# Performance work log

Hardware: AMD Instinct MI355X
Metric: run time of the kernel (lower is better)

The kernel has to match this reference:

```python
import jax, jax.numpy as jnp
import numpy as np

NEG_SLOPE = 0.2
NUM_GRAPHS = 256


def _gatv2(x, src, dst, n_nodes, Wl, Wr, att, bias):
    # PyG GATv2Conv (heads=1): e_ij = att . leaky_relu(Wl x_j + Wr x_i)
    xl = x @ Wl                      # [N, C]
    xr = x @ Wr                      # [N, C]
    e = jnp.dot(jax.nn.leaky_relu(xl[src] + xr[dst], NEG_SLOPE), att)  # [E]
    # segment softmax over incoming edges of each target node
    m = jax.ops.segment_max(e, dst, num_segments=n_nodes)
    m = jnp.where(jnp.isfinite(m), m, 0.0)
    p = jnp.exp(e - m[dst])
    denom = jax.ops.segment_sum(p, dst, num_segments=n_nodes)
    alpha = p / jnp.maximum(denom[dst], 1e-16)
    out = jax.ops.segment_sum(alpha[:, None] * xl[src], dst, num_segments=n_nodes)
    return out + bias


def _add_self_loops(edge_index, n_nodes):
    loops = jnp.arange(n_nodes, dtype=edge_index.dtype)
    src = jnp.concatenate([edge_index[0], loops])
    dst = jnp.concatenate([edge_index[1], loops])
    return src, dst


def setup_inputs() -> dict:
    key = jax.random.key(0)
    ks = jax.random.split(key, 12)
    N, F = 100000, 128
    E = 3200000
    x = jax.random.normal(ks[0], (N, F), dtype=jnp.float32)
    edge_index = jax.random.randint(ks[1], (2, E), 0, N, dtype=jnp.int32)
    batch = jnp.sort(jax.random.randint(ks[2], (N,), 0, NUM_GRAPHS, dtype=jnp.int32))
    def glorot(k, shape):
        lim = float(np.sqrt(6.0 / sum(shape)))
        return jax.random.uniform(k, shape, jnp.float32, -lim, lim)
    return {
        "x": x, "edge_index": edge_index, "batch": batch,
        "W1l": glorot(ks[3], (F, 16)), "W1r": glorot(ks[4], (F, 16)),
        "a1": glorot(ks[5], (16,)), "b1": jnp.zeros((16,), jnp.float32),
        "W2l": glorot(ks[6], (16, 8)), "W2r": glorot(ks[7], (16, 8)),
        "a2": glorot(ks[8], (8,)), "b2": jnp.zeros((8,), jnp.float32),
        "Wlin": glorot(ks[9], (8, 1)), "blin": jnp.zeros((1,), jnp.float32),
    }


def reference(x, edge_index, batch, W1l, W1r, a1, b1, W2l, W2r, a2, b2, Wlin, blin):
    n_nodes = x.shape[0]
    src, dst = _add_self_loops(edge_index, n_nodes)
    h = jax.nn.relu(_gatv2(x, src, dst, n_nodes, W1l, W1r, a1, b1))
    h = jax.nn.relu(_gatv2(h, src, dst, n_nodes, W2l, W2r, a2, b2))
    # dropout omitted (deterministic reference)
    sums = jax.ops.segment_sum(h, batch, num_segments=NUM_GRAPHS)
    cnts = jax.ops.segment_sum(jnp.ones((n_nodes,), h.dtype), batch, num_segments=NUM_GRAPHS)
    pooled = sums / jnp.maximum(cnts, 1.0)[:, None]   # [G, 8]
    return pooled @ Wlin + blin                        # [G, 1]
```

## Files before the change

### kernel.cpp

```cpp
#include <hip/hip_runtime.h>
#include <hip/hip_bf16.h>
#include <math.h>

#define NBLK 256
#define NBS  512

__device__ __forceinline__ unsigned bfr(float x) {
  unsigned u = __float_as_uint(x);
  return (u + 0x7fffu + ((u >> 16) & 1u)) >> 16;
}
__device__ __forceinline__ unsigned bfpk(float lo, float hi) {
  return (bfr(hi) << 16) | bfr(lo);
}
__device__ __forceinline__ float bflo(unsigned u) { return __uint_as_float(u << 16); }
__device__ __forceinline__ float bfhi(unsigned u) { return __uint_as_float(u & 0xffff0000u); }

__global__ __launch_bounds__(256) void k_bin_count(const int* __restrict__ ei,
    int E, int ET, int chunk, int* __restrict__ A) {
  __shared__ int lh[NBS];
  int t = threadIdx.x;
  lh[t] = 0; lh[t + 256] = 0;
  __syncthreads();
  int beg = blockIdx.x * chunk, end = min(beg + chunk, ET);
  for (int i = beg + t; i < end; i += 256) {
    int d = (i < E) ? ei[E + i] : (i - E);
    atomicAdd(&lh[d >> 8], 1);
  }
  __syncthreads();
  A[t * NBLK + blockIdx.x] = lh[t];
  A[(t + 256) * NBLK + blockIdx.x] = lh[t + 256];
}

__global__ void k_reduce(const int* __restrict__ a, int* bsum, int n) {
  int i = blockIdx.x * 256 + threadIdx.x;
  int v = (i < n) ? a[i] : 0;
  #pragma unroll
  for (int off = 32; off; off >>= 1) v += __shfl_down(v, off, 64);
  __shared__ int sh[4];
  if ((threadIdx.x & 63) == 0) sh[threadIdx.x >> 6] = v;
  __syncthreads();
  if (threadIdx.x == 0) bsum[blockIdx.x] = sh[0] + sh[1] + sh[2] + sh[3];
}

__global__ void k_scan_bsum(int* bsum, int nb) {
  __shared__ int sh[512];
  int t = threadIdx.x;
  int v = (t < nb) ? bsum[t] : 0;
  sh[t] = v; __syncthreads();
  for (int off = 1; off < 512; off <<= 1) {
    int add = (t >= off) ? sh[t - off] : 0;
    __syncthreads();
    sh[t] += add;
    __syncthreads();
  }
  if (t < nb) bsum[t] = sh[t] - v;
}

__global__ void k_scan_apply(int* A, const int* __restrict__ bsum, int n) {
  __shared__ int sh[256];
  int t = threadIdx.x; int i = blockIdx.x * 256 + t;
  int v = (i < n) ? A[i] : 0;
  sh[t] = v; __syncthreads();
  for (int off = 1; off < 256; off <<= 1) {
    int add = (t >= off) ? sh[t - off] : 0;
    __syncthreads();
    sh[t] += add;
    __syncthreads();
  }
  int excl = sh[t] - v + bsum[blockIdx.x];
  if (i < n) A[i] = excl;
  if (i == n - 1) A[n] = excl + v;
}

__global__ __launch_bounds__(256) void k_bin_scatter(const int* __restrict__ ei,
    int E, int ET, int chunk, const int* __restrict__ A, int* __restrict__ pairs) {
  __shared__ int cur[NBS];
  int t = threadIdx.x;
  cur[t]       = A[t * NBLK + blockIdx.x];
  cur[t + 256] = A[(t + 256) * NBLK + blockIdx.x];
  __syncthreads();
  int beg = blockIdx.x * chunk, end = min(beg + chunk, ET);
  for (int i = beg + t; i < end; i += 256) {
    int s, d;
    if (i < E) { s = ei[i]; d = ei[E + i]; } else { s = d = i - E; }
    int pos = atomicAdd(&cur[d >> 8], 1);
    pairs[pos] = (s << 8) | (d & 255);
  }
}

__global__ __launch_bounds__(256) void k_csr_build(const int* __restrict__ pairs,
    const int* __restrict__ A, int* __restrict__ csr_ptr, int* __restrict__ csr_src,
    int N, int NBu) {
  __shared__ int cnt[256];
  __shared__ int cur[256];
  __shared__ int sh[256];
  int b = blockIdx.x, t = threadIdx.x;
  int base = A[b * NBLK], endp = A[(b + 1) * NBLK];
  int node0 = b << 8;
  cnt[t] = 0;
  __syncthreads();
  for (int e = base + t; e < endp; e += 256)
    atomicAdd(&cnt[pairs[e] & 255], 1);
  __syncthreads();
  int v = cnt[t];
  sh[t] = v; __syncthreads();
  for (int off = 1; off < 256; off <<= 1) {
    int add = (t >= off) ? sh[t - off] : 0;
    __syncthreads();
    sh[t] += add;
    __syncthreads();
  }
  int excl = sh[t] - v;
  if (node0 + t < N) csr_ptr[node0 + t] = base + excl;
  cur[t] = base + excl;
  if (b == NBu - 1 && t == 0) csr_ptr[N] = endp;
  __syncthreads();
  for (int e = base + t; e < endp; e += 256) {
    int p = pairs[e];
    int pos = atomicAdd(&cur[p & 255], 1);
    csr_src[pos] = ((unsigned)p) >> 8;
  }
}

__global__ __launch_bounds__(256) void k_gemm1(const float* __restrict__ x,
    const float* __restrict__ Wl, const float* __restrict__ Wr,
    unsigned* __restrict__ xlb, float* __restrict__ xr, int n) {
  __shared__ float xs[64 * 132];
  __shared__ float Ws[128 * 32];
  int t = threadIdx.x;
  int r0 = blockIdx.x * 64;
  #pragma unroll
  for (int i = 0; i < 8; i++) {
    int idx = t + i * 256;
    int k = idx >> 4, c = idx & 15;
    Ws[k * 32 + c]      = Wl[idx];
    Ws[k * 32 + 16 + c] = Wr[idx];
  }
  #pragma unroll
  for (int i = 0; i < 8; i++) {
    int v = t + i * 256;
    int row = v >> 5;
    int col4 = v & 31;
    float4 val = make_float4(0.f, 0.f, 0.f, 0.f);
    if (r0 + row < n)
      val = reinterpret_cast<const float4*>(x)[(long)(r0 + row) * 32 + col4];
    float* dst = &xs[row * 132 + col4 * 4];
    dst[0] = val.x; dst[1] = val.y; dst[2] = val.z; dst[3] = val.w;
  }
  __syncthreads();
  int g = t >> 2;
  int sub = t & 3;
  float acc[8] = {0.f,0.f,0.f,0.f,0.f,0.f,0.f,0.f};
  #pragma unroll 4
  for (int k = 0; k < 128; k++) {
    float xv = xs[g * 132 + k];
    const float4* wp = reinterpret_cast<const float4*>(&Ws[k * 32 + sub * 8]);
    float4 w0 = wp[0], w1 = wp[1];
    acc[0] += xv * w0.x; acc[1] += xv * w0.y; acc[2] += xv * w0.z; acc[3] += xv * w0.w;
    acc[4] += xv * w1.x; acc[5] += xv * w1.y; acc[6] += xv * w1.z; acc[7] += xv * w1.w;
  }
  int row = r0 + g;
  if (row < n) {
    if (sub < 2) {
      uint4 pk;
      pk.x = bfpk(acc[0], acc[1]); pk.y = bfpk(acc[2], acc[3]);
      pk.z = bfpk(acc[4], acc[5]); pk.w = bfpk(acc[6], acc[7]);
      reinterpret_cast<uint4*>(xlb)[(long)row * 2 + sub] = pk;
    } else {
      float4* o4 = reinterpret_cast<float4*>(&xr[(long)row * 16 + (sub - 2) * 8]);
      o4[0] = make_float4(acc[0], acc[1], acc[2], acc[3]);
      o4[1] = make_float4(acc[4], acc[5], acc[6], acc[7]);
    }
  }
}

template<int CTRL>
__device__ __forceinline__ float dpp_mov(float x) {
  return __int_as_float(__builtin_amdgcn_update_dpp(0, __float_as_int(x), CTRL, 0xF, 0xF, true));
}
__device__ __forceinline__ float quad_sum(float x) {
  x += dpp_mov<0xB1>(x);
  x += dpp_mov<0x4E>(x);
  return x;
}
__device__ __forceinline__ float quad_max(float x) {
  x = fmaxf(x, dpp_mov<0xB1>(x));
  x = fmaxf(x, dpp_mov<0x4E>(x));
  return x;
}

__global__ __launch_bounds__(256) void k_edge1(const int* __restrict__ csr_ptr,
    const int* __restrict__ csr_src, const unsigned* __restrict__ xlb,
    const float* __restrict__ xr, const float* __restrict__ att,
    const float* __restrict__ bias, const float* __restrict__ W2l,
    const float* __restrict__ W2r, unsigned* __restrict__ xl2b,
    float* __restrict__ xr2, int n) {
  __shared__ float Ws[16 * 16];
  int t = threadIdx.x;
  if (t < 128) {
    int k = t >> 3, j = t & 7;
    Ws[k * 16 + j]     = W2l[t];
    Ws[k * 16 + 8 + j] = W2r[t];
  }
  __syncthreads();
  int node = blockIdx.x * 64 + (t >> 2);
  int sub = t & 3;
  if (node >= n) return;
  int beg = csr_ptr[node], end = csr_ptr[node + 1];
  float xrv[16], av[16], nu[16];
  const float4* xrp = reinterpret_cast<const float4*>(xr + (long)node * 16);
  #pragma unroll
  for (int q = 0; q < 4; q++) {
    float4 v = xrp[q];
    xrv[q*4] = v.x; xrv[q*4+1] = v.y; xrv[q*4+2] = v.z; xrv[q*4+3] = v.w;
  }
  #pragma unroll
  for (int c = 0; c < 16; c++) { av[c] = att[c]; nu[c] = 0.f; }
  float m = 0.f, s = 0.f;
  int i = beg + sub;
  uint4 ra, rb;
  if (i < end) {
    const uint4* p = reinterpret_cast<const uint4*>(xlb + (long)csr_src[i] * 8);
    ra = p[0]; rb = p[1];
  }
  while (i < end) {
    int nx = i + 4;
    uint4 na = ra, nb = rb;
    if (nx < end) {
      const uint4* p = reinterpret_cast<const uint4*>(xlb + (long)csr_src[nx] * 8);
      na = p[0]; nb = p[1];
    }
    unsigned uu[8] = {ra.x, ra.y, ra.z, ra.w, rb.x, rb.y, rb.z, rb.w};
    float xlv[16];
    #pragma unroll
    for (int k = 0; k < 8; k++) { xlv[2*k] = bflo(uu[k]); xlv[2*k+1] = bfhi(uu[k]); }
    float e1a = 0.f, e1b = 0.f, e2a = 0.f, e2b = 0.f;
    #pragma unroll
    for (int c = 0; c < 8; c++) {
      float za = xlv[c] + xrv[c];
      float zb = xlv[c + 8] + xrv[c + 8];
      e1a += av[c] * za;       e2a += av[c] * fabsf(za);
      e1b += av[c + 8] * zb;   e2b += av[c + 8] * fabsf(zb);
    }
    float e = 0.6f * (e1a + e1b) + 0.4f * (e2a + e2b);
    if (e > m + 25.f) {
      float sc = __expf(m - e);
      s *= sc;
      #pragma unroll
      for (int c = 0; c < 16; c++) nu[c] *= sc;
      m = e;
    }
    float pe = __expf(e - m);
    s += pe;
    #pragma unroll
    for (int c = 0; c < 16; c++) nu[c] += pe * xlv[c];
    ra = na; rb = nb; i = nx;
  }
  float M = quad_max(m);
  float sc = __expf(m - M);
  float S = quad_sum(s * sc);
  float o[16];
  #pragma unroll
  for (int c = 0; c < 16; c++) o[c] = quad_sum(nu[c] * sc);
  float inv = 1.f / fmaxf(S, 1e-16f);
  #pragma unroll
  for (int c = 0; c < 16; c++) o[c] = fmaxf(o[c] * inv + bias[c], 0.f);
  float r[4] = {0.f, 0.f, 0.f, 0.f};
  int j0 = sub * 4;
  #pragma unroll
  for (int k = 0; k < 16; k++) {
    float ok = o[k];
    const float* wk = &Ws[k * 16 + j0];
    r[0] += ok * wk[0]; r[1] += ok * wk[1]; r[2] += ok * wk[2]; r[3] += ok * wk[3];
  }
  if (sub < 2) {
    uint2 pk; pk.x = bfpk(r[0], r[1]); pk.y = bfpk(r[2], r[3]);
    reinterpret_cast<uint2*>(xl2b)[(long)node * 2 + sub] = pk;
  } else {
    reinterpret_cast<float4*>(xr2)[(long)node * 2 + (sub - 2)] =
        make_float4(r[0], r[1], r[2], r[3]);
  }
}

__global__ __launch_bounds__(256) void k_edge2(const int* __restrict__ csr_ptr,
    const int* __restrict__ csr_src, const unsigned* __restrict__ xlb,
    const float* __restrict__ xr, const float* __restrict__ att,
    const float* __restrict__ bias, float* __restrict__ out, int n) {
  int t = threadIdx.x;
  int node = blockIdx.x * 64 + (t >> 2);
  int sub = t & 3;
  if (node >= n) return;
  int beg = csr_ptr[node], end = csr_ptr[node + 1];
  float xrv[8], av[8], nu[8];
  const float4* xrp = reinterpret_cast<const float4*>(xr + (long)node * 8);
  {
    float4 v0 = xrp[0], v1 = xrp[1];
    xrv[0]=v0.x; xrv[1]=v0.y; xrv[2]=v0.z; xrv[3]=v0.w;
    xrv[4]=v1.x; xrv[5]=v1.y; xrv[6]=v1.z; xrv[7]=v1.w;
  }
  #pragma unroll
  for (int c = 0; c < 8; c++) { av[c] = att[c]; nu[c] = 0.f; }
  float m = 0.f, s = 0.f;
  int i = beg + sub;
  uint4 ra;
  if (i < end) ra = reinterpret_cast<const uint4*>(xlb)[csr_src[i]];
  while (i < end) {
    int nx = i + 4;
    uint4 na = ra;
    if (nx < end) na = reinterpret_cast<const uint4*>(xlb)[csr_src[nx]];
    unsigned uu[4] = {ra.x, ra.y, ra.z, ra.w};
    float xlv[8];
    #pragma unroll
    for (int k = 0; k < 4; k++) { xlv[2*k] = bflo(uu[k]); xlv[2*k+1] = bfhi(uu[k]); }
    float e1a = 0.f, e1b = 0.f, e2a = 0.f, e2b = 0.f;
    #pragma unroll
    for (int c = 0; c < 4; c++) {
      float za = xlv[c] + xrv[c];
      float zb = xlv[c + 4] + xrv[c + 4];
      e1a += av[c] * za;       e2a += av[c] * fabsf(za);
      e1b += av[c + 4] * zb;   e2b += av[c + 4] * fabsf(zb);
    }
    float e = 0.6f * (e1a + e1b) + 0.4f * (e2a + e2b);
    if (e > m + 25.f) {
      float sc = __expf(m - e);
      s *= sc;
      #pragma unroll
      for (int c = 0; c < 8; c++) nu[c] *= sc;
      m = e;
    }
    float pe = __expf(e - m);
    s += pe;
    #pragma unroll
    for (int c = 0; c < 8; c++) nu[c] += pe * xlv[c];
    ra = na; i = nx;
  }
  float M = quad_max(m);
  float sc = __expf(m - M);
  float S = quad_sum(s * sc);
  float o[8];
  #pragma unroll
  for (int c = 0; c < 8; c++) o[c] = quad_sum(nu[c] * sc);
  float inv = 1.f / fmaxf(S, 1e-16f);
  #pragma unroll
  for (int c = 0; c < 8; c++) o[c] = fmaxf(o[c] * inv + bias[c], 0.f);
  if (sub < 2) {
    float4* po = reinterpret_cast<float4*>(out + (long)node * 8 + sub * 4);
    *po = make_float4(o[sub*4], o[sub*4+1], o[sub*4+2], o[sub*4+3]);
  }
}

__global__ __launch_bounds__(256) void k_pool_final(const float* __restrict__ h,
    const int* __restrict__ batch, const float* __restrict__ Wlin,
    const float* __restrict__ blin, float* __restrict__ out, int n) {
  int g = blockIdx.x;
  int lo = 0, hi = n;
  while (lo < hi) { int mid = (lo + hi) >> 1; if (batch[mid] < g) lo = mid + 1; else hi = mid; }
  int beg = lo;
  hi = n;
  while (lo < hi) { int mid = (lo + hi) >> 1; if (batch[mid] < g + 1) lo = mid + 1; else hi = mid; }
  int end = lo;

  float w[8];
  #pragma unroll
  for (int c = 0; c < 8; c++) w[c] = Wlin[c];

  float acc = 0.f;
  int t = threadIdx.x;
  for (int i = beg + t; i < end; i += 256) {
    const float4* hp = reinterpret_cast<const float4*>(h + (long)i * 8);
    float4 v0 = hp[0], v1 = hp[1];
    acc += v0.x * w[0] + v0.y * w[1] + v0.z * w[2] + v0.w * w[3]
         + v1.x * w[4] + v1.y * w[5] + v1.z * w[6] + v1.w * w[7];
  }
  #pragma unroll
  for (int off = 32; off; off >>= 1) acc += __shfl_down(acc, off, 64);
  __shared__ float sh[4];
  if ((t & 63) == 0) sh[t >> 6] = acc;
  __syncthreads();
  if (t == 0) {
    float total = sh[0] + sh[1] + sh[2] + sh[3];
    float cnt = (float)(end - beg);
    out[g] = total / fmaxf(cnt, 1.f) + blin[0];
  }
}

extern "C" void kernel_launch(void* const* d_in, const int* in_sizes, int n_in,
                              void* d_out, int out_size, void* d_ws, size_t ws_size,
                              hipStream_t stream) {
  (void)n_in; (void)ws_size;
  const float* x    = (const float*)d_in[0];
  const int*   ei   = (const int*)d_in[1];
  const int*   batch= (const int*)d_in[2];
  const float* W1l  = (const float*)d_in[3];
  const float* W1r  = (const float*)d_in[4];
  const float* a1   = (const float*)d_in[5];
  const float* b1   = (const float*)d_in[6];
  const float* W2l  = (const float*)d_in[7];
  const float* W2r  = (const float*)d_in[8];
  const float* a2   = (const float*)d_in[9];
  const float* b2   = (const float*)d_in[10];
  const float* Wlin = (const float*)d_in[11];
  const float* blin = (const float*)d_in[12];
  float* out = (float*)d_out;

  int N = in_sizes[0] / 128;
  int E = in_sizes[1] / 2;
  int G = out_size;
  int ET = E + N;
  int NBu = (N + 255) >> 8;
  int chunk = (ET + NBLK - 1) / NBLK;
  int nA = NBS * NBLK;

  char* ws = (char*)d_ws;
  size_t off = 0;
  auto alloc = [&](size_t bytes) {
    void* p = ws + off; off = (off + bytes + 255) & ~(size_t)255; return p;
  };
  int* csr_ptr = (int*)alloc((size_t)(N + 1) * 4);
  int* A       = (int*)alloc((size_t)(nA + 1) * 4);
  int* bsum    = (int*)alloc(512 * 4);
  int* csr_src = (int*)alloc((size_t)ET * 4);
  size_t featBytes = (size_t)N * (32 + 64 + 16 + 32 + 32);
  size_t pairBytes = (size_t)ET * 4;
  char* u = (char*)alloc(pairBytes > featBytes ? pairBytes : featBytes);
  int* pairs = (int*)u;
  unsigned* xl1b = (unsigned*)u;
  float* xr1     = (float*)(u + (size_t)N * 32);
  unsigned* xl2b = (unsigned*)(u + (size_t)N * 96);
  float* xr2     = (float*)(u + (size_t)N * 112);
  float* h2      = (float*)(u + (size_t)N * 144);

  k_bin_count<<<NBLK, 256, 0, stream>>>(ei, E, ET, chunk, A);
  k_reduce<<<(nA + 255) / 256, 256, 0, stream>>>(A, bsum, nA);
  k_scan_bsum<<<1, 512, 0, stream>>>(bsum, (nA + 255) / 256);
  k_scan_apply<<<(nA + 255) / 256, 256, 0, stream>>>(A, bsum, nA);
  k_bin_scatter<<<NBLK, 256, 0, stream>>>(ei, E, ET, chunk, A, pairs);
  k_csr_build<<<NBu, 256, 0, stream>>>(pairs, A, csr_ptr, csr_src, N, NBu);
  k_gemm1<<<(N + 63) / 64, 256, 0, stream>>>(x, W1l, W1r, xl1b, xr1, N);
  k_edge1<<<(N + 63) / 64, 256, 0, stream>>>(csr_ptr, csr_src, xl1b, xr1, a1, b1,
                                             W2l, W2r, xl2b, xr2, N);
  k_edge2<<<(N + 63) / 64, 256, 0, stream>>>(csr_ptr, csr_src, xl2b, xr2, a2, b2, h2, N);
  k_pool_final<<<G, 256, 0, stream>>>(h2, batch, Wlin, blin, out, N);
}
```

Baseline: 181.7 us.

## Deepen gather prefetch in edge kernels, widen binning blocks and vectorize scans

```diff
diff --git a/kernel.cpp b/kernel.cpp
--- a/kernel.cpp
+++ b/kernel.cpp
@@ -2,7 +2,7 @@
 #include <hip/hip_bf16.h>
 #include <math.h>
 
-#define NBLK 256
+#define NBLK 1024
 #define NBS  512
 
 __device__ __forceinline__ unsigned bfr(float x) {
@@ -31,15 +31,22 @@
   A[(t + 256) * NBLK + blockIdx.x] = lh[t + 256];
 }
 
-__global__ void k_reduce(const int* __restrict__ a, int* bsum, int n) {
-  int i = blockIdx.x * 256 + threadIdx.x;
-  int v = (i < n) ? a[i] : 0;
+__global__ void k_reduce4(const int* __restrict__ a, int* bsum, int n) {
+  int t = threadIdx.x;
+  int base = blockIdx.x * 1024 + t * 4;
+  int v = 0;
+  if (base + 3 < n) {
+    int4 q = *reinterpret_cast<const int4*>(a + base);
+    v = q.x + q.y + q.z + q.w;
+  } else {
+    for (int k = 0; k < 4; k++) if (base + k < n) v += a[base + k];
+  }
   #pragma unroll
   for (int off = 32; off; off >>= 1) v += __shfl_down(v, off, 64);
   __shared__ int sh[4];
-  if ((threadIdx.x & 63) == 0) sh[threadIdx.x >> 6] = v;
-  __syncthreads();
-  if (threadIdx.x == 0) bsum[blockIdx.x] = sh[0] + sh[1] + sh[2] + sh[3];
+  if ((t & 63) == 0) sh[t >> 6] = v;
+  __syncthreads();
+  if (t == 0) bsum[blockIdx.x] = sh[0] + sh[1] + sh[2] + sh[3];
 }
 
 __global__ void k_scan_bsum(int* bsum, int nb) {
@@ -56,20 +63,24 @@
   if (t < nb) bsum[t] = sh[t] - v;
 }
 
-__global__ void k_scan_apply(int* A, const int* __restrict__ bsum, int n) {
+__global__ void k_scan_apply4(int* A, const int* __restrict__ bsum, int n) {
   __shared__ int sh[256];
-  int t = threadIdx.x; int i = blockIdx.x * 256 + t;
-  int v = (i < n) ? A[i] : 0;
-  sh[t] = v; __syncthreads();
+  int t = threadIdx.x;
+  int base = blockIdx.x * 1024 + t * 4;
+  int4 q = *reinterpret_cast<const int4*>(A + base);
+  int tsum = q.x + q.y + q.z + q.w;
+  sh[t] = tsum; __syncthreads();
   for (int off = 1; off < 256; off <<= 1) {
     int add = (t >= off) ? sh[t - off] : 0;
     __syncthreads();
     sh[t] += add;
     __syncthreads();
   }
-  int excl = sh[t] - v + bsum[blockIdx.x];
-  if (i < n) A[i] = excl;
-  if (i == n - 1) A[n] = excl + v;
+  int excl = sh[t] - tsum + bsum[blockIdx.x];
+  int4 w;
+  w.x = excl; w.y = w.x + q.x; w.z = w.y + q.y; w.w = w.z + q.z;
+  *reinterpret_cast<int4*>(A + base) = w;
+  if (base + 4 == n) A[n] = w.w + q.w;
 }
 
 __global__ __launch_bounds__(256) void k_bin_scatter(const int* __restrict__ ei,
@@ -88,7 +99,7 @@
   }
 }
 
-__global__ __launch_bounds__(256) void k_csr_build(const int* __restrict__ pairs,
+__global__ __launch_bounds__(512) void k_csr_build(const int* __restrict__ pairs,
     const int* __restrict__ A, int* __restrict__ csr_ptr, int* __restrict__ csr_src,
     int N, int NBu) {
   __shared__ int cnt[256];
@@ -97,25 +108,28 @@
   int b = blockIdx.x, t = threadIdx.x;
   int base = A[b * NBLK], endp = A[(b + 1) * NBLK];
   int node0 = b << 8;
-  cnt[t] = 0;
-  __syncthreads();
-  for (int e = base + t; e < endp; e += 256)
+  if (t < 256) cnt[t] = 0;
+  __syncthreads();
+  for (int e = base + t; e < endp; e += 512)
     atomicAdd(&cnt[pairs[e] & 255], 1);
   __syncthreads();
-  int v = cnt[t];
-  sh[t] = v; __syncthreads();
+  int v = (t < 256) ? cnt[t] : 0;
+  if (t < 256) sh[t] = v;
+  __syncthreads();
   for (int off = 1; off < 256; off <<= 1) {
-    int add = (t >= off) ? sh[t - off] : 0;
+    int add = (t >= off && t < 256) ? sh[t - off] : 0;
     __syncthreads();
-    sh[t] += add;
+    if (t < 256) sh[t] += add;
     __syncthreads();
   }
-  int excl = sh[t] - v;
-  if (node0 + t < N) csr_ptr[node0 + t] = base + excl;
-  cur[t] = base + excl;
+  if (t < 256) {
+    int excl = sh[t] - v;
+    if (node0 + t < N) csr_ptr[node0 + t] = base + excl;
+    cur[t] = base + excl;
+  }
   if (b == NBu - 1 && t == 0) csr_ptr[N] = endp;
   __syncthreads();
-  for (int e = base + t; e < endp; e += 256) {
+  for (int e = base + t; e < endp; e += 512) {
     int p = pairs[e];
     int pos = atomicAdd(&cur[p & 255], 1);
     csr_src[pos] = ((unsigned)p) >> 8;
@@ -217,19 +231,8 @@
   #pragma unroll
   for (int c = 0; c < 16; c++) { av[c] = att[c]; nu[c] = 0.f; }
   float m = 0.f, s = 0.f;
-  int i = beg + sub;
-  uint4 ra, rb;
-  if (i < end) {
-    const uint4* p = reinterpret_cast<const uint4*>(xlb + (long)csr_src[i] * 8);
-    ra = p[0]; rb = p[1];
-  }
-  while (i < end) {
-    int nx = i + 4;
-    uint4 na = ra, nb = rb;
-    if (nx < end) {
-      const uint4* p = reinterpret_cast<const uint4*>(xlb + (long)csr_src[nx] * 8);
-      na = p[0]; nb = p[1];
-    }
+
+  auto PROCESS = [&](const uint4& ra, const uint4& rb) {
     unsigned uu[8] = {ra.x, ra.y, ra.z, ra.w, rb.x, rb.y, rb.z, rb.w};
     float xlv[16];
     #pragma unroll
@@ -254,8 +257,46 @@
     s += pe;
     #pragma unroll
     for (int c = 0; c < 16; c++) nu[c] += pe * xlv[c];
-    ra = na; rb = nb; i = nx;
-  }
+  };
+
+  int i = beg + sub;
+  int i3 = i + 12;
+  int x3 = 0;
+  uint4 a0, b0, a1, b1, a2, b2;
+  if (i < end) {
+    int x0 = csr_src[i];
+    const uint4* p = reinterpret_cast<const uint4*>(xlb + (long)x0 * 8);
+    a0 = p[0]; b0 = p[1];
+  }
+  if (i + 4 < end) {
+    int x1 = csr_src[i + 4];
+    const uint4* p = reinterpret_cast<const uint4*>(xlb + (long)x1 * 8);
+    a1 = p[0]; b1 = p[1];
+  }
+  if (i + 8 < end) {
+    int x2 = csr_src[i + 8];
+    const uint4* p = reinterpret_cast<const uint4*>(xlb + (long)x2 * 8);
+    a2 = p[0]; b2 = p[1];
+  }
+  if (i3 < end) x3 = csr_src[i3];
+
+  #define STEP1(AA, BB)                                                         \
+    if (i >= end) break;                                                        \
+    PROCESS(AA, BB);                                                            \
+    if (i3 < end) {                                                             \
+      const uint4* p = reinterpret_cast<const uint4*>(xlb + (long)x3 * 8);      \
+      AA = p[0]; BB = p[1];                                                     \
+    }                                                                           \
+    i += 4; i3 += 4;                                                            \
+    if (i3 < end) x3 = csr_src[i3];
+
+  for (;;) {
+    STEP1(a0, b0)
+    STEP1(a1, b1)
+    STEP1(a2, b2)
+  }
+  #undef STEP1
+
   float M = quad_max(m);
   float sc = __expf(m - M);
   float S = quad_sum(s * sc);
@@ -301,13 +342,8 @@
   #pragma unroll
   for (int c = 0; c < 8; c++) { av[c] = att[c]; nu[c] = 0.f; }
   float m = 0.f, s = 0.f;
-  int i = beg + sub;
-  uint4 ra;
-  if (i < end) ra = reinterpret_cast<const uint4*>(xlb)[csr_src[i]];
-  while (i < end) {
-    int nx = i + 4;
-    uint4 na = ra;
-    if (nx < end) na = reinterpret_cast<const uint4*>(xlb)[csr_src[nx]];
+
+  auto PROCESS = [&](const uint4& ra) {
     unsigned uu[4] = {ra.x, ra.y, ra.z, ra.w};
     float xlv[8];
     #pragma unroll
@@ -332,8 +368,31 @@
     s += pe;
     #pragma unroll
     for (int c = 0; c < 8; c++) nu[c] += pe * xlv[c];
-    ra = na; i = nx;
-  }
+  };
+
+  int i = beg + sub;
+  int i3 = i + 12;
+  int x3 = 0;
+  uint4 r0, r1, r2;
+  if (i < end)     r0 = reinterpret_cast<const uint4*>(xlb)[csr_src[i]];
+  if (i + 4 < end) r1 = reinterpret_cast<const uint4*>(xlb)[csr_src[i + 4]];
+  if (i + 8 < end) r2 = reinterpret_cast<const uint4*>(xlb)[csr_src[i + 8]];
+  if (i3 < end) x3 = csr_src[i3];
+
+  #define STEP2(RR)                                                   \
+    if (i >= end) break;                                              \
+    PROCESS(RR);                                                      \
+    if (i3 < end) RR = reinterpret_cast<const uint4*>(xlb)[x3];       \
+    i += 4; i3 += 4;                                                  \
+    if (i3 < end) x3 = csr_src[i3];
+
+  for (;;) {
+    STEP2(r0)
+    STEP2(r1)
+    STEP2(r2)
+  }
+  #undef STEP2
+
   float M = quad_max(m);
   float sc = __expf(m - M);
   float S = quad_sum(s * sc);
@@ -431,11 +490,11 @@
   float* h2      = (float*)(u + (size_t)N * 144);
 
   k_bin_count<<<NBLK, 256, 0, stream>>>(ei, E, ET, chunk, A);
-  k_reduce<<<(nA + 255) / 256, 256, 0, stream>>>(A, bsum, nA);
-  k_scan_bsum<<<1, 512, 0, stream>>>(bsum, (nA + 255) / 256);
-  k_scan_apply<<<(nA + 255) / 256, 256, 0, stream>>>(A, bsum, nA);
+  k_reduce4<<<nA / 1024, 256, 0, stream>>>(A, bsum, nA);
+  k_scan_bsum<<<1, 512, 0, stream>>>(bsum, nA / 1024);
+  k_scan_apply4<<<nA / 1024, 256, 0, stream>>>(A, bsum, nA);
   k_bin_scatter<<<NBLK, 256, 0, stream>>>(ei, E, ET, chunk, A, pairs);
-  k_csr_build<<<NBu, 256, 0, stream>>>(pairs, A, csr_ptr, csr_src, N, NBu);
+  k_csr_build<<<NBu, 512, 0, stream>>>(pairs, A, csr_ptr, csr_src, N, NBu);
   k_gemm1<<<(N + 63) / 64, 256, 0, stream>>>(x, W1l, W1r, xl1b, xr1, N);
   k_edge1<<<(N + 63) / 64, 256, 0, stream>>>(csr_ptr, csr_src, xl1b, xr1, a1, b1,
                                              W2l, W2r, xl2b, xr2, N);
```

Result: no change. 179.3 us (-1.3%).
